# Optimization experiments

Measured on AMD Instinct MI355X. Metric: run time of the kernel, lower is better.

The kernel has to match this reference:

```python
import jax, jax.numpy as jnp
import numpy as np
import math

N_NODES = 100000
N_EDGES = 1_600_000
NFEAT = 512
NHID = 128
NLAYERS = 6
NCLASS = 64


def setup_inputs() -> dict:
    key = jax.random.key(0)
    ks = jax.random.split(key, 8)
    x = jax.random.normal(ks[0], (N_NODES, NFEAT), jnp.float32)
    rows = jax.random.randint(ks[1], (N_EDGES,), 0, N_NODES, dtype=jnp.int32)
    cols = jax.random.randint(ks[2], (N_EDGES,), 0, N_NODES, dtype=jnp.int32)
    # normalized-adjacency-like edge weights
    vals = jax.random.uniform(ks[3], (N_EDGES,), jnp.float32) * (1.0 / 16.0)
    s = 1.0 / math.sqrt(NHID)  # reset_parameters: uniform(-1/sqrt(out_features), ...)
    W0 = jax.random.uniform(ks[4], (NFEAT, NHID), jnp.float32, minval=-s, maxval=s)
    Wh = jax.random.uniform(ks[5], (NLAYERS - 1, NHID, NHID), jnp.float32, minval=-s, maxval=s)
    Wfc = jax.random.normal(ks[6], (NHID * NLAYERS, NCLASS), jnp.float32) * 0.02
    bfc = jnp.zeros((NCLASS,), jnp.float32)
    return {"x": x, "rows": rows, "cols": cols, "vals": vals,
            "W0": W0, "Wh": Wh, "Wfc": Wfc, "bfc": bfc}


def _spmm(rows, cols, vals, h, n):
    # sparse [n,n] @ h : gather source rows, scale by edge weight, scatter-add to dest
    return jax.ops.segment_sum(vals[:, None] * h[cols], rows, num_segments=n)


def reference(x, rows, cols, vals, W0, Wh, Wfc, bfc):
    n = x.shape[0]
    # conv0: relu(spmm(A, x @ W0))  (inference: no dropout, no skip-gate)
    h = jax.nn.relu(_spmm(rows, cols, vals, x @ W0, n))
    hiddens = [h]
    for i in range(Wh.shape[0]):
        h = jax.nn.relu(_spmm(rows, cols, vals, h @ Wh[i], n))
        hiddens.append(h)
    logits = jnp.concatenate(hiddens, axis=-1) @ Wfc + bfc
    return jax.nn.log_softmax(logits, axis=1)
```

## Files before the change

kernel.cpp:

```cpp
#include <hip/hip_runtime.h>
#include <hip/hip_bf16.h>
#include <cstdint>
#include <cstddef>

static constexpr int NFEAT   = 512;
static constexpr int NHID    = 128;
static constexpr int NLAYERS = 6;
static constexpr int NCLASS  = 64;

typedef __bf16 bf16x8 __attribute__((ext_vector_type(8)));
typedef float  floatx4 __attribute__((ext_vector_type(4)));

static __device__ __forceinline__ uint16_t f2bf(float v){
    __hip_bfloat16 h = __float2bfloat16(v);
    return *reinterpret_cast<uint16_t*>(&h);
}

__global__ void k_sniff(const uint16_t* __restrict__ x, int nwords, uint32_t* __restrict__ flag){
    int i = blockIdx.x*256 + threadIdx.x;
    if (i < nwords){
        uint16_t w = x[i];
        if ((w & 0x7F80u) == 0x7F80u) atomicOr(flag, 1u);
    }
}

__global__ void k_sentinel(uint16_t* out, int nel){
    int i = blockIdx.x*256 + threadIdx.x;
    if (i < nel) out[i] = 0x3E00u;
}

__global__ void k_hist(const int* __restrict__ rows, uint32_t* __restrict__ deg, int nE){
    int e = blockIdx.x*256 + threadIdx.x;
    if (e < nE) atomicAdd(&deg[rows[e]], 1u);
}

__global__ __launch_bounds__(1024) void k_scan1(const uint32_t* __restrict__ deg,
                                                uint32_t* __restrict__ row_start,
                                                uint32_t* __restrict__ partial, int n){
    __shared__ uint32_t sh[1024];
    int tid = threadIdx.x;
    int i = blockIdx.x*1024 + tid;
    uint32_t v = (i < n) ? deg[i] : 0u;
    sh[tid] = v; __syncthreads();
    for (int off = 1; off < 1024; off <<= 1){
        uint32_t t = (tid >= off) ? sh[tid-off] : 0u;
        __syncthreads();
        sh[tid] += t;
        __syncthreads();
    }
    if (i < n) row_start[i+1] = sh[tid];
    if (tid == 1023) partial[blockIdx.x] = sh[1023];
}

__global__ __launch_bounds__(128) void k_scan2(uint32_t* partial, int nb){
    __shared__ uint32_t sh[128];
    int tid = threadIdx.x;
    uint32_t v = (tid < nb) ? partial[tid] : 0u;
    sh[tid] = v; __syncthreads();
    for (int off = 1; off < 128; off <<= 1){
        uint32_t t = (tid >= off) ? sh[tid-off] : 0u;
        __syncthreads();
        sh[tid] += t;
        __syncthreads();
    }
    if (tid < nb) partial[tid] = sh[tid] - v;
}

__global__ __launch_bounds__(1024) void k_scan3(const uint32_t* __restrict__ deg,
                                                uint32_t* __restrict__ row_start,
                                                const uint32_t* __restrict__ partial,
                                                uint32_t* __restrict__ bcur,
                                                uint32_t* __restrict__ cursor, int n){
    int i = blockIdx.x*1024 + threadIdx.x;
    if (i < n){
        uint32_t rs = row_start[i+1] + partial[blockIdx.x];
        row_start[i+1] = rs;
        uint32_t start = rs - deg[i];
        cursor[i] = start;
        if ((i & 255) == 0) bcur[i >> 8] = start;
        if (i == 0) row_start[0] = 0u;
    }
}

__global__ void k_scatter(const int* __restrict__ rows, const int* __restrict__ cols,
                          const void* __restrict__ vals,
                          uint32_t* __restrict__ cursor, uint2* __restrict__ ep, int nE,
                          const uint32_t* __restrict__ flags){
    int e = blockIdx.x*256 + threadIdx.x;
    if (e < nE){
        int r = rows[e];
        uint32_t pos = atomicAdd(&cursor[r], 1u);
        float v;
        if (flags[0]) v = ((const float*)vals)[e];
        else          v = __bfloat162float(((const __hip_bfloat16*)vals)[e]);
        ep[pos] = make_uint2((uint32_t)cols[e], __float_as_uint(v));
    }
}

__global__ __launch_bounds__(256) void k_bin(
    const int* __restrict__ rows, const int* __restrict__ cols,
    const void* __restrict__ vals,
    uint32_t* __restrict__ bcur,
    uint2* __restrict__ epb, uint8_t* __restrict__ rloc,
    int nE, int nbuck, int epb_per_block,
    const uint32_t* __restrict__ flags)
{
    __shared__ uint32_t h[512];
    const int tid = threadIdx.x;
    const int e0 = blockIdx.x * epb_per_block;
    int e1 = e0 + epb_per_block; if (e1 > nE) e1 = nE;

    for (int b = tid; b < nbuck; b += 256) h[b] = 0u;
    __syncthreads();
    for (int e = e0 + tid; e < e1; e += 256){
        int r = rows[e];
        atomicAdd(&h[r >> 8], 1u);
    }
    __syncthreads();
    for (int b = tid; b < nbuck; b += 256){
        uint32_t c = h[b];
        h[b] = c ? atomicAdd(&bcur[b], c) : 0u;
    }
    __syncthreads();
    const int fp32 = (int)flags[0];
    for (int e = e0 + tid; e < e1; e += 256){
        int r = rows[e];
        uint32_t pos = atomicAdd(&h[r >> 8], 1u);
        float v;
        if (fp32) v = ((const float*)vals)[e];
        else      v = __bfloat162float(((const __hip_bfloat16*)vals)[e]);
        epb[pos] = make_uint2((uint32_t)cols[e], __float_as_uint(v));
        rloc[pos] = (uint8_t)(r & 255);
    }
}

__global__ __launch_bounds__(256) void k_csr(
    const uint32_t* __restrict__ row_start,
    const uint2* __restrict__ epb, const uint8_t* __restrict__ rloc,
    uint2* __restrict__ ep, int n)
{
    __shared__ uint32_t curs[256];
    const int b = blockIdx.x;
    const int r0 = b << 8;
    const int tid = threadIdx.x;
    const int r = r0 + tid;
    curs[tid] = (r < n) ? row_start[r] : 0u;
    __syncthreads();
    int rend = r0 + 256; if (rend > n) rend = n;
    const uint32_t s = row_start[r0];
    const uint32_t e = row_start[rend];
    for (uint32_t i = s + tid; i < e; i += 256){
        uint2 rec = epb[i];
        uint32_t rl = rloc[i];
        uint32_t pos = atomicAdd(&curs[rl], 1u);
        ep[pos] = rec;
    }
}

__global__ void k_transpose_all(const void* __restrict__ W0, const void* __restrict__ Wh,
                                const void* __restrict__ Wfc,
                                uint16_t* __restrict__ W0t, uint16_t* __restrict__ Wht,
                                uint16_t* __restrict__ Wfct,
                                const uint32_t* __restrict__ flags)
{
    const int idx = blockIdx.x*256 + threadIdx.x;
    const int T0 = NFEAT*NHID;
    const int T1 = (NLAYERS-1)*NHID*NHID;
    const int T2 = NLAYERS*NHID*NCLASS;
    const int fp32 = (int)flags[0];
    if (idx < T0){
        uint16_t w = fp32 ? f2bf(((const float*)W0)[idx]) : ((const uint16_t*)W0)[idx];
        int k = idx / NHID, nn = idx - k*NHID;
        W0t[nn*NFEAT + k] = w;
    } else if (idx < T0 + T1){
        int j = idx - T0;
        uint16_t w = fp32 ? f2bf(((const float*)Wh)[j]) : ((const uint16_t*)Wh)[j];
        int l = j / (NHID*NHID); int jj = j - l*(NHID*NHID);
        int k = jj / NHID, nn = jj - k*NHID;
        Wht[l*NHID*NHID + nn*NHID + k] = w;
    } else if (idx < T0 + T1 + T2){
        int j = idx - T0 - T1;
        uint16_t w = fp32 ? f2bf(((const float*)Wfc)[j]) : ((const uint16_t*)Wfc)[j];
        int k = j / NCLASS, nn = j - k*NCLASS;
        Wfct[nn*(NLAYERS*NHID) + k] = w;
    }
}

template<int NTILES, int MODE>
__global__ __launch_bounds__(256) void k_gemm(
    const void* __restrict__ Aany, int lda,
    const uint16_t* __restrict__ Bt, int ldb, int K, int Mwaves,
    uint16_t* __restrict__ Cb, float* __restrict__ Cf,
    const uint32_t* __restrict__ flagsp)
{
    __shared__ uint16_t lds[NTILES*16*40];
    const int tid  = threadIdx.x;
    const int lane = tid & 63;
    const int gw   = blockIdx.x*4 + (tid >> 6);
    const bool active = gw < Mwaves;
    const int m = lane & 15, quad = lane >> 4;
    const long row0 = (long)gw * 16;
    const int afp32 = flagsp ? (int)flagsp[0] : 0;
    const uint16_t* A16 = (const uint16_t*)Aany;
    const float*    A32 = (const float*)Aany;

    floatx4 acc[NTILES];
#pragma unroll
    for (int i = 0; i < NTILES; i++) acc[i] = (floatx4){0.f,0.f,0.f,0.f};

    for (int kk = 0; kk < K; kk += 32){
        for (int idx = tid; idx < NTILES*16*4; idx += 256){
            int nn = idx >> 2, c = idx & 3;
            *(bf16x8*)&lds[nn*40 + c*8] = *(const bf16x8*)&Bt[(long)nn*ldb + kk + c*8];
        }
        __syncthreads();
        if (active){
            bf16x8 a;
            if (afp32){
                const float* p = &A32[(row0 + m)*lda + kk + quad*8];
                float4 f0 = *(const float4*)p;
                float4 f1 = *(const float4*)(p + 4);
                a[0]=(__bf16)f0.x; a[1]=(__bf16)f0.y; a[2]=(__bf16)f0.z; a[3]=(__bf16)f0.w;
                a[4]=(__bf16)f1.x; a[5]=(__bf16)f1.y; a[6]=(__bf16)f1.z; a[7]=(__bf16)f1.w;
            } else {
                a = *(const bf16x8*)&A16[(row0 + m)*lda + kk + quad*8];
            }
#pragma unroll
            for (int nt = 0; nt < NTILES; nt++){
                bf16x8 b = *(const bf16x8*)&lds[(nt*16 + m)*40 + quad*8];
                acc[nt] = __builtin_amdgcn_mfma_f32_16x16x32_bf16(a, b, acc[nt], 0, 0, 0);
            }
        }
        __syncthreads();
    }
    if (active){
#pragma unroll
        for (int nt = 0; nt < NTILES; nt++){
#pragma unroll
            for (int r = 0; r < 4; r++){
                long row = row0 + quad*4 + r;
                int  col = nt*16 + m;
                float v = acc[nt][r];
                if (MODE == 1) Cf[row*(NTILES*16) + col] += v;
                else           Cb[row*(NTILES*16) + col] = f2bf(v);
            }
        }
    }
}

__global__ __launch_bounds__(256) void k_gemm_final(
    const uint16_t* __restrict__ A,
    const uint16_t* __restrict__ Bt, int ldb, int Mwaves,
    const float* __restrict__ logits, const void* __restrict__ bias,
    void* __restrict__ outp, const uint32_t* __restrict__ flags)
{
    __shared__ uint16_t lds[4*16*40];
    const int tid  = threadIdx.x;
    const int lane = tid & 63;
    const int gw   = blockIdx.x*4 + (tid >> 6);
    const bool active = gw < Mwaves;
    const int m = lane & 15, quad = lane >> 4;
    const long row0 = (long)gw * 16;

    floatx4 acc[4];
#pragma unroll
    for (int i = 0; i < 4; i++) acc[i] = (floatx4){0.f,0.f,0.f,0.f};

    for (int kk = 0; kk < 128; kk += 32){
        for (int idx = tid; idx < 4*16*4; idx += 256){
            int nn = idx >> 2, c = idx & 3;
            *(bf16x8*)&lds[nn*40 + c*8] = *(const bf16x8*)&Bt[(long)nn*ldb + kk + c*8];
        }
        __syncthreads();
        if (active){
            bf16x8 a = *(const bf16x8*)&A[(row0 + m)*128 + kk + quad*8];
#pragma unroll
            for (int nt = 0; nt < 4; nt++){
                bf16x8 b = *(const bf16x8*)&lds[(nt*16 + m)*40 + quad*8];
                acc[nt] = __builtin_amdgcn_mfma_f32_16x16x32_bf16(a, b, acc[nt], 0, 0, 0);
            }
        }
        __syncthreads();
    }
    if (active){
        const int fp32 = (int)flags[0];
        float b[4];
#pragma unroll
        for (int nt = 0; nt < 4; nt++){
            int col = nt*16 + m;
            b[nt] = fp32 ? ((const float*)bias)[col]
                         : __bfloat162float(((const __hip_bfloat16*)bias)[col]);
        }
#pragma unroll
        for (int r = 0; r < 4; r++){
            long row = row0 + quad*4 + r;
            float v[4];
#pragma unroll
            for (int nt = 0; nt < 4; nt++){
                int col = nt*16 + m;
                v[nt] = logits[row*64 + col] + acc[nt][r] + b[nt];
            }
            float mx = fmaxf(fmaxf(v[0],v[1]), fmaxf(v[2],v[3]));
#pragma unroll
            for (int off = 1; off < 16; off <<= 1) mx = fmaxf(mx, __shfl_xor(mx, off));
            float sum = __expf(v[0]-mx)+__expf(v[1]-mx)+__expf(v[2]-mx)+__expf(v[3]-mx);
#pragma unroll
            for (int off = 1; off < 16; off <<= 1) sum += __shfl_xor(sum, off);
            float ls = mx + __logf(sum);
#pragma unroll
            for (int nt = 0; nt < 4; nt++){
                int col = nt*16 + m;
                float rr = v[nt] - ls;
                if (fp32) ((float*)outp)[row*64 + col] = rr;
                else      ((uint16_t*)outp)[row*64 + col] = f2bf(rr);
            }
        }
    }
}

__global__ __launch_bounds__(256) void k_gemm_fused(
    const uint16_t* __restrict__ A,
    const uint16_t* __restrict__ B1t,
    const uint16_t* __restrict__ B2t, int ldb2,
    uint16_t* __restrict__ C1, float* __restrict__ C2, int nchunks,
    int store_c2)
{
    __shared__ uint16_t lds[(128+64)*132];
    const int tid = threadIdx.x, lane = tid & 63;
    for (int idx = tid; idx < 128*16; idx += 256){
        int nn = idx >> 4, c = idx & 15;
        *(bf16x8*)&lds[nn*132 + c*8] = *(const bf16x8*)&B1t[nn*128 + c*8];
    }
    for (int idx = tid; idx < 64*16; idx += 256){
        int nn = idx >> 4, c = idx & 15;
        *(bf16x8*)&lds[(128+nn)*132 + c*8] = *(const bf16x8*)&B2t[(long)nn*ldb2 + c*8];
    }
    __syncthreads();

    const int m = lane & 15, quad = lane >> 4;
    const int nw = gridDim.x * 4;
    for (int chunk = blockIdx.x*4 + (tid >> 6); chunk < nchunks; chunk += nw){
        const long row0 = (long)chunk * 16;
        const uint16_t* Arow = &A[(row0 + m)*128 + quad*8];
        bf16x8 a[4];
#pragma unroll
        for (int ks = 0; ks < 4; ks++) a[ks] = *(const bf16x8*)&Arow[ks*32];

        floatx4 acc1[8], acc2[4];
#pragma unroll
        for (int i = 0; i < 8; i++) acc1[i] = (floatx4){0.f,0.f,0.f,0.f};
#pragma unroll
        for (int i = 0; i < 4; i++) acc2[i] = (floatx4){0.f,0.f,0.f,0.f};

#pragma unroll
        for (int ks = 0; ks < 4; ks++){
            const int kk = ks*32 + quad*8;
#pragma unroll
            for (int nt = 0; nt < 8; nt++){
                bf16x8 b = *(const bf16x8*)&lds[(nt*16 + m)*132 + kk];
                acc1[nt] = __builtin_amdgcn_mfma_f32_16x16x32_bf16(a[ks], b, acc1[nt], 0, 0, 0);
            }
#pragma unroll
            for (int nt = 0; nt < 4; nt++){
                bf16x8 b = *(const bf16x8*)&lds[(128 + nt*16 + m)*132 + kk];
                acc2[nt] = __builtin_amdgcn_mfma_f32_16x16x32_bf16(a[ks], b, acc2[nt], 0, 0, 0);
            }
        }
#pragma unroll
        for (int nt = 0; nt < 8; nt++){
#pragma unroll
            for (int r = 0; r < 4; r++){
                long row = row0 + quad*4 + r;
                int  col = nt*16 + m;
                float v  = acc1[nt][r];
                float vn = __shfl_xor(v, 1);
                if ((m & 1) == 0){
                    uint32_t pk = (uint32_t)f2bf(v) | ((uint32_t)f2bf(vn) << 16);
                    *(uint32_t*)&C1[row*128 + col] = pk;
                }
            }
        }
#pragma unroll
        for (int nt = 0; nt < 4; nt++){
#pragma unroll
            for (int r = 0; r < 4; r++){
                long row = row0 + quad*4 + r;
                int  col = nt*16 + m;
                float v  = acc2[nt][r];
                float vn = __shfl_xor(v, 1);
                if ((m & 1) == 0){
                    float2* p = (float2*)&C2[row*64 + col];
                    if (store_c2){
                        float2 o; o.x = v; o.y = vn; *p = o;
                    } else {
                        float2 o = *p;
                        o.x += v; o.y += vn;
                        *p = o;
                    }
                }
            }
        }
    }
}

__global__ __launch_bounds__(256) void k_spmm(
    const uint2* __restrict__ ep, const uint32_t* __restrict__ row_start,
    const uint32_t* __restrict__ tmp, uint16_t* __restrict__ out, int n)
{
    int t = blockIdx.x*256 + threadIdx.x;
    int gw = t >> 6, lane = t & 63;
    if (gw >= n) return;
    uint32_t s = row_start[gw], e = row_start[gw+1];
    const int q  = lane >> 4;
    const int fl = lane & 15;
    float acc[8];
#pragma unroll
    for (int i = 0; i < 8; i++) acc[i] = 0.f;

#define ACC8(P, V) { \
    acc[0] = fmaf(V, __uint_as_float((P).x << 16), acc[0]); \
    acc[1] = fmaf(V, __uint_as_float((P).x & 0xffff0000u), acc[1]); \
    acc[2] = fmaf(V, __uint_as_float((P).y << 16), acc[2]); \
    acc[3] = fmaf(V, __uint_as_float((P).y & 0xffff0000u), acc[3]); \
    acc[4] = fmaf(V, __uint_as_float((P).z << 16), acc[4]); \
    acc[5] = fmaf(V, __uint_as_float((P).z & 0xffff0000u), acc[5]); \
    acc[6] = fmaf(V, __uint_as_float((P).w << 16), acc[6]); \
    acc[7] = fmaf(V, __uint_as_float((P).w & 0xffff0000u), acc[7]); }

#pragma unroll 2
    for (uint32_t j = s; j < e; j += 8){
        uint32_t i0 = j + q;
        uint32_t i1 = j + q + 4;
        uint2 d0 = (i0 < e) ? ep[i0] : make_uint2(0u, 0u);
        uint2 d1 = (i1 < e) ? ep[i1] : make_uint2(0u, 0u);
        float v0 = __uint_as_float(d0.y);
        float v1 = __uint_as_float(d1.y);
        uint4 p0 = *(const uint4*)&tmp[(size_t)(d0.x << 6) + fl*4];
        uint4 p1 = *(const uint4*)&tmp[(size_t)(d1.x << 6) + fl*4];
        ACC8(p0, v0); ACC8(p1, v1);
    }
#undef ACC8

#pragma unroll
    for (int i = 0; i < 8; i++){
        acc[i] += __shfl_xor(acc[i], 16);
        acc[i] += __shfl_xor(acc[i], 32);
    }
    if (q == 0){
        uint32_t w0 = (uint32_t)f2bf(fmaxf(acc[0],0.f)) | ((uint32_t)f2bf(fmaxf(acc[1],0.f)) << 16);
        uint32_t w1 = (uint32_t)f2bf(fmaxf(acc[2],0.f)) | ((uint32_t)f2bf(fmaxf(acc[3],0.f)) << 16);
        uint32_t w2 = (uint32_t)f2bf(fmaxf(acc[4],0.f)) | ((uint32_t)f2bf(fmaxf(acc[5],0.f)) << 16);
        uint32_t w3 = (uint32_t)f2bf(fmaxf(acc[6],0.f)) | ((uint32_t)f2bf(fmaxf(acc[7],0.f)) << 16);
        uint4 o = make_uint4(w0, w1, w2, w3);
        *(uint4*)&out[(size_t)gw*128 + fl*8] = o;
    }
}

extern "C" void kernel_launch(void* const* d_in, const int* in_sizes, int n_in,
                              void* d_out, int out_size, void* d_ws, size_t ws_size,
                              hipStream_t stream){
    const void* x    = d_in[0];
    const int* rows  = (const int*)d_in[1];
    const int* cols  = (const int*)d_in[2];
    const void* vals = d_in[3];
    const void* W0   = d_in[4];
    const void* Wh   = d_in[5];
    const void* Wfc  = d_in[6];
    const void* bfc  = d_in[7];

    const int n  = in_sizes[0] / NFEAT;
    const int nE = in_sizes[1];

    char* ws = (char*)d_ws;
    size_t off = 0;
    auto alloc = [&](size_t bytes)->char*{
        char* p = ws + off;
        off = (off + bytes + 255) & ~(size_t)255;
        return p;
    };
    uint32_t* flags     = (uint32_t*)alloc(256);
    uint32_t* deg       = (uint32_t*)alloc((size_t)n*4);
    uint32_t* row_start = (uint32_t*)alloc(((size_t)n+1)*4);
    uint32_t* cursor    = (uint32_t*)alloc((size_t)n*4);
    uint32_t* partial   = (uint32_t*)alloc(512);
    uint32_t* bcur      = (uint32_t*)alloc(2048);
    uint2*    ep        = (uint2*)   alloc((size_t)nE*8);
    uint16_t* W0t       = (uint16_t*)alloc((size_t)NFEAT*NHID*2);
    uint16_t* Wht       = (uint16_t*)alloc((size_t)(NLAYERS-1)*NHID*NHID*2);
    uint16_t* Wfct      = (uint16_t*)alloc((size_t)NCLASS*NLAYERS*NHID*2);
    uint16_t* tmp       = (uint16_t*)alloc((size_t)n*NHID*2);
    uint16_t* hbuf      = (uint16_t*)alloc((size_t)n*NHID*2);
    float*    logits    = (float*)   alloc((size_t)n*NCLASS*4);

    if (ws_size < off){
        k_sentinel<<<(out_size+255)/256, 256, 0, stream>>>((uint16_t*)d_out, out_size);
        return;
    }

    hipMemsetAsync(flags, 0, 4, stream);
    const int NW = 1 << 20;
    k_sniff<<<NW/256, 256, 0, stream>>>((const uint16_t*)x, NW, flags);

    const int scanBlocks = (n + 1023)/1024;
    hipMemsetAsync(deg, 0, (size_t)n*4, stream);
    k_hist<<<(nE+255)/256, 256, 0, stream>>>(rows, deg, nE);
    k_scan1<<<scanBlocks, 1024, 0, stream>>>(deg, row_start, partial, n);
    k_scan2<<<1, 128, 0, stream>>>(partial, scanBlocks);
    k_scan3<<<scanBlocks, 1024, 0, stream>>>(deg, row_start, partial, bcur, cursor, n);

    const int TTOT = NFEAT*NHID + (NLAYERS-1)*NHID*NHID + NLAYERS*NHID*NCLASS;
    k_transpose_all<<<(TTOT+255)/256, 256, 0, stream>>>(W0, Wh, Wfc, W0t, Wht, Wfct, flags);

    const int nbuck = (n + 255) >> 8;
    if (nbuck <= 512 && (size_t)n*NHID*2 >= (size_t)nE*9){
        uint2*   epb  = (uint2*)tmp;
        uint8_t* rloc = (uint8_t*)tmp + (size_t)nE*8;
        const int EPB = 2048;
        k_bin<<<(nE+EPB-1)/EPB, 256, 0, stream>>>(rows, cols, vals, bcur, epb, rloc,
                                                  nE, nbuck, EPB, flags);
        k_csr<<<nbuck, 256, 0, stream>>>(row_start, epb, rloc, ep, n);
    } else {
        k_scatter<<<(nE+255)/256, 256, 0, stream>>>(rows, cols, vals, cursor, ep, nE, flags);
    }

    const int Mwaves = n/16;
    const int gemmBlocks = (Mwaves + 3)/4;
    const int rowBlocks  = (n*64 + 255)/256;
    const int fusedBlocks = 768;

    k_gemm<8,0><<<gemmBlocks, 256, 0, stream>>>(x, NFEAT, W0t, NFEAT, NFEAT, Mwaves, tmp, nullptr, flags);
    k_spmm<<<rowBlocks, 256, 0, stream>>>(ep, row_start, (const uint32_t*)tmp, hbuf, n);
    for (int l = 1; l < NLAYERS; l++){
        k_gemm_fused<<<fusedBlocks, 256, 0, stream>>>(hbuf, Wht + (l-1)*NHID*NHID,
                                                      Wfct + (l-1)*NHID, NLAYERS*NHID,
                                                      tmp, logits, Mwaves, (l == 1) ? 1 : 0);
        k_spmm<<<rowBlocks, 256, 0, stream>>>(ep, row_start, (const uint32_t*)tmp, hbuf, n);
    }
    k_gemm_final<<<gemmBlocks, 256, 0, stream>>>(hbuf, Wfct + (NLAYERS-1)*NHID, NLAYERS*NHID,
                                                 Mwaves, logits, bfc, d_out, flags);
}
```

Baseline: 1.142 ms.

## Feature-slice layout and chunked LDS-accumulating SpMM per 16-column slice

Changes the hidden and tmp buffers to a sliced layout of 8 column groups of 16 features, so each slice of the gather source is about 3.2 MB and more likely to stay in cache. The SpMM is rewritten so a block handles a 512-row chunk for one slice. Threads take contiguous edge ranges, keep a running row sum and flush it into LDS with shared atomics, using a new per-edge local-row index array written during CSR build. The GEMMs are updated to read and write the sliced layout. This trades the one-wave-per-row 128-wide gather for more L2 locality, at the cost of LDS atomics, load imbalance and extra rl16 traffic.

```diff
diff --git a/kernel.cpp b/kernel.cpp
--- a/kernel.cpp
+++ b/kernel.cpp
@@ -7,6 +7,7 @@
 static constexpr int NHID    = 128;
 static constexpr int NLAYERS = 6;
 static constexpr int NCLASS  = 64;
+static constexpr int CHUNK   = 512;
 
 typedef __bf16 bf16x8 __attribute__((ext_vector_type(8)));
 typedef float  floatx4 __attribute__((ext_vector_type(4)));
@@ -15,6 +16,8 @@
     __hip_bfloat16 h = __float2bfloat16(v);
     return *reinterpret_cast<uint16_t*>(&h);
 }
+static __device__ __forceinline__ float bflo(uint32_t w){ return __uint_as_float(w << 16); }
+static __device__ __forceinline__ float bfhi(uint32_t w){ return __uint_as_float(w & 0xffff0000u); }
 
 __global__ void k_sniff(const uint16_t* __restrict__ x, int nwords, uint32_t* __restrict__ flag){
     int i = blockIdx.x*256 + threadIdx.x;
@@ -97,6 +100,15 @@
     }
 }
 
+__global__ void k_rl16(const uint32_t* __restrict__ row_start, uint16_t* __restrict__ rl16, int n){
+    int r = blockIdx.x*256 + threadIdx.x;
+    if (r < n){
+        uint32_t s = row_start[r], e = row_start[r+1];
+        uint16_t v = (uint16_t)(r & (CHUNK-1));
+        for (uint32_t i = s; i < e; ++i) rl16[i] = v;
+    }
+}
+
 __global__ __launch_bounds__(256) void k_bin(
     const int* __restrict__ rows, const int* __restrict__ cols,
     const void* __restrict__ vals,
@@ -137,7 +149,7 @@
 __global__ __launch_bounds__(256) void k_csr(
     const uint32_t* __restrict__ row_start,
     const uint2* __restrict__ epb, const uint8_t* __restrict__ rloc,
-    uint2* __restrict__ ep, int n)
+    uint2* __restrict__ ep, uint16_t* __restrict__ rl16, int n)
 {
     __shared__ uint32_t curs[256];
     const int b = blockIdx.x;
@@ -149,11 +161,13 @@
     int rend = r0 + 256; if (rend > n) rend = n;
     const uint32_t s = row_start[r0];
     const uint32_t e = row_start[rend];
+    const uint32_t hi = (uint32_t)(b & 1) << 8;
     for (uint32_t i = s + tid; i < e; i += 256){
         uint2 rec = epb[i];
         uint32_t rl = rloc[i];
         uint32_t pos = atomicAdd(&curs[rl], 1u);
         ep[pos] = rec;
+        rl16[pos] = (uint16_t)(hi | rl);
     }
 }
 
@@ -186,11 +200,11 @@
     }
 }
 
-template<int NTILES, int MODE>
-__global__ __launch_bounds__(256) void k_gemm(
+template<int NTILES>
+__global__ __launch_bounds__(256) void k_gemm0(
     const void* __restrict__ Aany, int lda,
-    const uint16_t* __restrict__ Bt, int ldb, int K, int Mwaves,
-    uint16_t* __restrict__ Cb, float* __restrict__ Cf,
+    const uint16_t* __restrict__ Bt, int ldb, int K, int Mwaves, long NN,
+    uint16_t* __restrict__ Cb,
     const uint32_t* __restrict__ flagsp)
 {
     __shared__ uint16_t lds[NTILES*16*40];
@@ -239,17 +253,14 @@
 #pragma unroll
             for (int r = 0; r < 4; r++){
                 long row = row0 + quad*4 + r;
-                int  col = nt*16 + m;
-                float v = acc[nt][r];
-                if (MODE == 1) Cf[row*(NTILES*16) + col] += v;
-                else           Cb[row*(NTILES*16) + col] = f2bf(v);
+                Cb[((long)nt*NN + row)*16 + m] = f2bf(acc[nt][r]);
             }
         }
     }
 }
 
 __global__ __launch_bounds__(256) void k_gemm_final(
-    const uint16_t* __restrict__ A,
+    const uint16_t* __restrict__ A, long NN,
     const uint16_t* __restrict__ Bt, int ldb, int Mwaves,
     const float* __restrict__ logits, const void* __restrict__ bias,
     void* __restrict__ outp, const uint32_t* __restrict__ flags)
@@ -273,7 +284,8 @@
         }
         __syncthreads();
         if (active){
-            bf16x8 a = *(const bf16x8*)&A[(row0 + m)*128 + kk + quad*8];
+            const long sl = (kk >> 4) + (quad >> 1);
+            bf16x8 a = *(const bf16x8*)&A[(sl*NN + row0 + m)*16 + (quad & 1)*8];
 #pragma unroll
             for (int nt = 0; nt < 4; nt++){
                 bf16x8 b = *(const bf16x8*)&lds[(nt*16 + m)*40 + quad*8];
@@ -319,7 +331,7 @@
 }
 
 __global__ __launch_bounds__(256) void k_gemm_fused(
-    const uint16_t* __restrict__ A,
+    const uint16_t* __restrict__ A, long NN,
     const uint16_t* __restrict__ B1t,
     const uint16_t* __restrict__ B2t, int ldb2,
     uint16_t* __restrict__ C1, float* __restrict__ C2, int nchunks,
@@ -341,10 +353,12 @@
     const int nw = gridDim.x * 4;
     for (int chunk = blockIdx.x*4 + (tid >> 6); chunk < nchunks; chunk += nw){
         const long row0 = (long)chunk * 16;
-        const uint16_t* Arow = &A[(row0 + m)*128 + quad*8];
         bf16x8 a[4];
 #pragma unroll
-        for (int ks = 0; ks < 4; ks++) a[ks] = *(const bf16x8*)&Arow[ks*32];
+        for (int ks = 0; ks < 4; ks++){
+            const long sl = ks*2 + (quad >> 1);
+            a[ks] = *(const bf16x8*)&A[(sl*NN + row0 + m)*16 + (quad & 1)*8];
+        }
 
         floatx4 acc1[8], acc2[4];
 #pragma unroll
@@ -371,12 +385,11 @@
 #pragma unroll
             for (int r = 0; r < 4; r++){
                 long row = row0 + quad*4 + r;
-                int  col = nt*16 + m;
                 float v  = acc1[nt][r];
                 float vn = __shfl_xor(v, 1);
                 if ((m & 1) == 0){
                     uint32_t pk = (uint32_t)f2bf(v) | ((uint32_t)f2bf(vn) << 16);
-                    *(uint32_t*)&C1[row*128 + col] = pk;
+                    *(uint32_t*)&C1[((long)nt*NN + row)*16 + m] = pk;
                 }
             }
         }
@@ -403,56 +416,78 @@
     }
 }
 
-__global__ __launch_bounds__(256) void k_spmm(
-    const uint2* __restrict__ ep, const uint32_t* __restrict__ row_start,
-    const uint32_t* __restrict__ tmp, uint16_t* __restrict__ out, int n)
-{
-    int t = blockIdx.x*256 + threadIdx.x;
-    int gw = t >> 6, lane = t & 63;
-    if (gw >= n) return;
-    uint32_t s = row_start[gw], e = row_start[gw+1];
-    const int q  = lane >> 4;
-    const int fl = lane & 15;
-    float acc[8];
-#pragma unroll
-    for (int i = 0; i < 8; i++) acc[i] = 0.f;
-
-#define ACC8(P, V) { \
-    acc[0] = fmaf(V, __uint_as_float((P).x << 16), acc[0]); \
-    acc[1] = fmaf(V, __uint_as_float((P).x & 0xffff0000u), acc[1]); \
-    acc[2] = fmaf(V, __uint_as_float((P).y << 16), acc[2]); \
-    acc[3] = fmaf(V, __uint_as_float((P).y & 0xffff0000u), acc[3]); \
-    acc[4] = fmaf(V, __uint_as_float((P).z << 16), acc[4]); \
-    acc[5] = fmaf(V, __uint_as_float((P).z & 0xffff0000u), acc[5]); \
-    acc[6] = fmaf(V, __uint_as_float((P).w << 16), acc[6]); \
-    acc[7] = fmaf(V, __uint_as_float((P).w & 0xffff0000u), acc[7]); }
-
-#pragma unroll 2
-    for (uint32_t j = s; j < e; j += 8){
-        uint32_t i0 = j + q;
-        uint32_t i1 = j + q + 4;
-        uint2 d0 = (i0 < e) ? ep[i0] : make_uint2(0u, 0u);
-        uint2 d1 = (i1 < e) ? ep[i1] : make_uint2(0u, 0u);
-        float v0 = __uint_as_float(d0.y);
-        float v1 = __uint_as_float(d1.y);
-        uint4 p0 = *(const uint4*)&tmp[(size_t)(d0.x << 6) + fl*4];
-        uint4 p1 = *(const uint4*)&tmp[(size_t)(d1.x << 6) + fl*4];
-        ACC8(p0, v0); ACC8(p1, v1);
-    }
-#undef ACC8
-
-#pragma unroll
-    for (int i = 0; i < 8; i++){
-        acc[i] += __shfl_xor(acc[i], 16);
-        acc[i] += __shfl_xor(acc[i], 32);
-    }
-    if (q == 0){
-        uint32_t w0 = (uint32_t)f2bf(fmaxf(acc[0],0.f)) | ((uint32_t)f2bf(fmaxf(acc[1],0.f)) << 16);
-        uint32_t w1 = (uint32_t)f2bf(fmaxf(acc[2],0.f)) | ((uint32_t)f2bf(fmaxf(acc[3],0.f)) << 16);
-        uint32_t w2 = (uint32_t)f2bf(fmaxf(acc[4],0.f)) | ((uint32_t)f2bf(fmaxf(acc[5],0.f)) << 16);
-        uint32_t w3 = (uint32_t)f2bf(fmaxf(acc[6],0.f)) | ((uint32_t)f2bf(fmaxf(acc[7],0.f)) << 16);
-        uint4 o = make_uint4(w0, w1, w2, w3);
-        *(uint4*)&out[(size_t)gw*128 + fl*8] = o;
+__global__ __launch_bounds__(256) void k_spmm_split(
+    const uint2* __restrict__ ep, const uint16_t* __restrict__ rl16,
+    const uint32_t* __restrict__ row_start,
+    const uint32_t* __restrict__ tmp, uint32_t* __restrict__ hbuf,
+    int n, long NN, int nch, int half)
+{
+    __shared__ float acc[CHUNK*17];
+    const int tid = threadIdx.x;
+    const int B = blockIdx.x;
+    const int x = B & 7;
+    const int j = B >> 3;
+    const int ph = j / half;
+    const int slice = (x >> 1) + 4*ph;
+    const int chunk = 2*(j - ph*half) + (x & 1);
+    if (chunk >= nch) return;
+    const int r0 = chunk * CHUNK;
+    int nr = n - r0; if (nr > CHUNK) nr = CHUNK;
+
+    for (int i = tid; i < CHUNK*17; i += 256) acc[i] = 0.f;
+    __syncthreads();
+
+    const uint32_t s0   = row_start[r0];
+    const uint32_t send = row_start[r0 + nr];
+    const uint32_t cnt  = send - s0;
+    const uint32_t len  = (cnt + 255) >> 8;
+    uint32_t e0 = s0 + (uint32_t)tid * len;
+    uint32_t e1 = e0 + len; if (e1 > send) e1 = send;
+
+    const uint32_t* tsl = tmp + (size_t)slice * NN * 8;
+
+    int cur = -1;
+    float f[16];
+#pragma unroll
+    for (int k = 0; k < 16; k++) f[k] = 0.f;
+
+    for (uint32_t e = e0; e < e1; ++e){
+        uint2 d = ep[e];
+        int rl = (int)rl16[e];
+        float v = __uint_as_float(d.y);
+        if (rl != cur){
+            if (cur >= 0){
+#pragma unroll
+                for (int k = 0; k < 16; k++) atomicAdd(&acc[cur*17 + k], f[k]);
+            }
+            cur = rl;
+#pragma unroll
+            for (int k = 0; k < 16; k++) f[k] = 0.f;
+        }
+        const uint4* tp = (const uint4*)(tsl + (size_t)d.x * 8);
+        uint4 pa = tp[0];
+        uint4 pb = tp[1];
+        f[0]  = fmaf(v, bflo(pa.x), f[0]);  f[1]  = fmaf(v, bfhi(pa.x), f[1]);
+        f[2]  = fmaf(v, bflo(pa.y), f[2]);  f[3]  = fmaf(v, bfhi(pa.y), f[3]);
+        f[4]  = fmaf(v, bflo(pa.z), f[4]);  f[5]  = fmaf(v, bfhi(pa.z), f[5]);
+        f[6]  = fmaf(v, bflo(pa.w), f[6]);  f[7]  = fmaf(v, bfhi(pa.w), f[7]);
+        f[8]  = fmaf(v, bflo(pb.x), f[8]);  f[9]  = fmaf(v, bfhi(pb.x), f[9]);
+        f[10] = fmaf(v, bflo(pb.y), f[10]); f[11] = fmaf(v, bfhi(pb.y), f[11]);
+        f[12] = fmaf(v, bflo(pb.z), f[12]); f[13] = fmaf(v, bfhi(pb.z), f[13]);
+        f[14] = fmaf(v, bflo(pb.w), f[14]); f[15] = fmaf(v, bfhi(pb.w), f[15]);
+    }
+    if (cur >= 0){
+#pragma unroll
+        for (int k = 0; k < 16; k++) atomicAdd(&acc[cur*17 + k], f[k]);
+    }
+    __syncthreads();
+
+    uint32_t* hsl = hbuf + (size_t)slice * NN * 8;
+    for (int idx = tid; idx < nr*8; idx += 256){
+        int rr = idx >> 3, fp = idx & 7;
+        float a0 = fmaxf(acc[rr*17 + fp*2],     0.f);
+        float a1 = fmaxf(acc[rr*17 + fp*2 + 1], 0.f);
+        hsl[(size_t)(r0 + rr)*8 + fp] = (uint32_t)f2bf(a0) | ((uint32_t)f2bf(a1) << 16);
     }
 }
 
@@ -485,11 +520,14 @@
     uint32_t* partial   = (uint32_t*)alloc(512);
     uint32_t* bcur      = (uint32_t*)alloc(2048);
     uint2*    ep        = (uint2*)   alloc((size_t)nE*8);
+    uint16_t* rl16      = (uint16_t*)alloc((size_t)nE*2);
     uint16_t* W0t       = (uint16_t*)alloc((size_t)NFEAT*NHID*2);
     uint16_t* Wht       = (uint16_t*)alloc((size_t)(NLAYERS-1)*NHID*NHID*2);
     uint16_t* Wfct      = (uint16_t*)alloc((size_t)NCLASS*NLAYERS*NHID*2);
-    uint16_t* tmp       = (uint16_t*)alloc((size_t)n*NHID*2);
-    uint16_t* hbuf      = (uint16_t*)alloc((size_t)n*NHID*2);
+    const int Mwaves = n/16;
+    const long NN = (long)Mwaves * 16;
+    uint16_t* tmp       = (uint16_t*)alloc((size_t)NN*NHID*2);
+    uint16_t* hbuf      = (uint16_t*)alloc((size_t)NN*NHID*2);
     float*    logits    = (float*)   alloc((size_t)n*NCLASS*4);
 
     if (ws_size < off){
@@ -512,30 +550,34 @@
     k_transpose_all<<<(TTOT+255)/256, 256, 0, stream>>>(W0, Wh, Wfc, W0t, Wht, Wfct, flags);
 
     const int nbuck = (n + 255) >> 8;
-    if (nbuck <= 512 && (size_t)n*NHID*2 >= (size_t)nE*9){
+    if (nbuck <= 512 && (size_t)NN*NHID*2 >= (size_t)nE*9){
         uint2*   epb  = (uint2*)tmp;
         uint8_t* rloc = (uint8_t*)tmp + (size_t)nE*8;
         const int EPB = 2048;
         k_bin<<<(nE+EPB-1)/EPB, 256, 0, stream>>>(rows, cols, vals, bcur, epb, rloc,
                                                   nE, nbuck, EPB, flags);
-        k_csr<<<nbuck, 256, 0, stream>>>(row_start, epb, rloc, ep, n);
+        k_csr<<<nbuck, 256, 0, stream>>>(row_start, epb, rloc, ep, rl16, n);
     } else {
         k_scatter<<<(nE+255)/256, 256, 0, stream>>>(rows, cols, vals, cursor, ep, nE, flags);
-    }
-
-    const int Mwaves = n/16;
+        k_rl16<<<(n+255)/256, 256, 0, stream>>>(row_start, rl16, n);
+    }
+
     const int gemmBlocks = (Mwaves + 3)/4;
-    const int rowBlocks  = (n*64 + 255)/256;
     const int fusedBlocks = 768;
-
-    k_gemm<8,0><<<gemmBlocks, 256, 0, stream>>>(x, NFEAT, W0t, NFEAT, NFEAT, Mwaves, tmp, nullptr, flags);
-    k_spmm<<<rowBlocks, 256, 0, stream>>>(ep, row_start, (const uint32_t*)tmp, hbuf, n);
+    const int nch  = (n + CHUNK - 1) / CHUNK;
+    const int half = (nch + 1) / 2;
+    const int spmmGrid = 16 * half;
+
+    k_gemm0<8><<<gemmBlocks, 256, 0, stream>>>(x, NFEAT, W0t, NFEAT, NFEAT, Mwaves, NN, tmp, flags);
+    k_spmm_split<<<spmmGrid, 256, 0, stream>>>(ep, rl16, row_start, (const uint32_t*)tmp,
+                                               (uint32_t*)hbuf, n, NN, nch, half);
     for (int l = 1; l < NLAYERS; l++){
-        k_gemm_fused<<<fusedBlocks, 256, 0, stream>>>(hbuf, Wht + (l-1)*NHID*NHID,
+        k_gemm_fused<<<fusedBlocks, 256, 0, stream>>>(hbuf, NN, Wht + (l-1)*NHID*NHID,
                                                       Wfct + (l-1)*NHID, NLAYERS*NHID,
                                                       tmp, logits, Mwaves, (l == 1) ? 1 : 0);
-        k_spmm<<<rowBlocks, 256, 0, stream>>>(ep, row_start, (const uint32_t*)tmp, hbuf, n);
-    }
-    k_gemm_final<<<gemmBlocks, 256, 0, stream>>>(hbuf, Wfct + (NLAYERS-1)*NHID, NLAYERS*NHID,
+        k_spmm_split<<<spmmGrid, 256, 0, stream>>>(ep, rl16, row_start, (const uint32_t*)tmp,
+                                                   (uint32_t*)hbuf, n, NN, nch, half);
+    }
+    k_gemm_final<<<gemmBlocks, 256, 0, stream>>>(hbuf, NN, Wfct + (NLAYERS-1)*NHID, NLAYERS*NHID,
                                                  Mwaves, logits, bfc, d_out, flags);
 }
```

Result: slower. 3.551 ms (+210.8%).
